# Optimization experiments

Measured on AMD Instinct MI355X. Metric: run time of the kernel, lower is better.

## Reference

```python
import jax, jax.numpy as jnp
import numpy as np

N_NODES = 100000
K_HOPS = 3  # PyG TAGConv default


def _gcn_norm(edge_index, num_nodes):
    # Symmetric normalization WITHOUT self-loops (TAGConv default).
    row, col = edge_index[0], edge_index[1]
    ones = jnp.ones(row.shape[0], dtype=jnp.float32)
    deg = jax.ops.segment_sum(ones, col, num_segments=num_nodes)
    dinv = jnp.where(deg > 0, jax.lax.rsqrt(jnp.maximum(deg, 1.0)), 0.0)
    return dinv[row] * dinv[col]


def _tagconv(x, row, col, norm, W, b, num_nodes):
    # out = Linear(concat_{k=0..K} (D^-1/2 A D^-1/2)^k x)
    xs = [x]
    h = x
    for _ in range(K_HOPS):
        h = jax.ops.segment_sum(norm[:, None] * h[row], col, num_segments=num_nodes)
        xs.append(h)
    return jnp.concatenate(xs, axis=-1) @ W.T + b


def setup_inputs() -> dict:
    key = jax.random.key(0)
    k1, k2, k3, k4, k5 = jax.random.split(key, 5)
    in_c, hid_c, out_c = 128, 128, 128
    n_edges = 1600000
    x = jax.random.normal(k1, (N_NODES, in_c), dtype=jnp.float32)
    edge_index = jax.random.randint(k2, (2, n_edges), 0, N_NODES, dtype=jnp.int64)
    s1 = 1.0 / np.sqrt(in_c * (K_HOPS + 1))
    s2 = 1.0 / np.sqrt(hid_c * (K_HOPS + 1))
    W1 = jax.random.normal(k3, (hid_c, in_c * (K_HOPS + 1)), dtype=jnp.float32) * s1
    b1 = jnp.zeros((hid_c,), dtype=jnp.float32)
    W2 = jax.random.normal(k4, (out_c, hid_c * (K_HOPS + 1)), dtype=jnp.float32) * s2
    b2 = jnp.zeros((out_c,), dtype=jnp.float32)
    return {"x": x, "edge_index": edge_index, "W1": W1, "b1": b1, "W2": W2, "b2": b2}


def reference(x, edge_index, W1, b1, W2, b2):
    row, col = edge_index[0], edge_index[1]
    norm = _gcn_norm(edge_index, N_NODES)  # [E]
    h = jax.nn.relu(_tagconv(x, row, col, norm, W1, b1, N_NODES))
    out = _tagconv(h, row, col, norm, W2, b2, N_NODES)
    return out.reshape(-1)  # original: x.view(n_nodes * out_channels)
```

## Files before the change

### kernel.cpp

```cpp
#include <hip/hip_runtime.h>
#include <hip/hip_fp16.h>

#define FEAT 128
#define BSH 8
#define BSZ 256
#define NBMAX 400
#define ABLK 4096
#define CAP 6144

typedef _Float16 half_t;
typedef _Float16 half4 __attribute__((ext_vector_type(4)));
typedef _Float16 half8 __attribute__((ext_vector_type(8)));
typedef float float4v __attribute__((ext_vector_type(4)));

__global__ void binit_kernel(int* __restrict__ gcur, int NB) {
    int b = blockIdx.x * blockDim.x + threadIdx.x;
    if (b < NB) gcur[b * 16] = b * CAP;
}

__global__ __launch_bounds__(256) void bucketA_kernel(const int* __restrict__ row,
                                                      const int* __restrict__ col,
                                                      int* __restrict__ gcur,
                                                      long long* __restrict__ tmp,
                                                      int E, int NB) {
    __shared__ int hist[NBMAX];
    __shared__ int gbase[NBMAX];
    int t = threadIdx.x;
    int base = blockIdx.x * ABLK;
    for (int i = t; i < NB; i += 256) hist[i] = 0;
    __syncthreads();
    int r[16], c[16];
#pragma unroll
    for (int j = 0; j < 16; ++j) {
        int e = base + j * 256 + t;
        if (e < E) {
            r[j] = __builtin_nontemporal_load(row + e);
            c[j] = __builtin_nontemporal_load(col + e);
            atomicAdd(&hist[c[j] >> BSH], 1);
        } else c[j] = -1;
    }
    __syncthreads();
    for (int b = t; b < NB; b += 256) {
        int cnt = hist[b];
        if (cnt > 0) gbase[b] = atomicAdd(&gcur[b * 16], cnt);
    }
    __syncthreads();
    for (int i = t; i < NB; i += 256) hist[i] = 0;
    __syncthreads();
#pragma unroll
    for (int j = 0; j < 16; ++j) {
        if (c[j] >= 0) {
            int b = c[j] >> BSH;
            int lpos = atomicAdd(&hist[b], 1);
            long long pk = ((long long)(unsigned)c[j] << 32) | (unsigned)r[j];
            tmp[gbase[b] + lpos] = pk;
        }
    }
}

__global__ __launch_bounds__(512) void bscan_kernel(const int* __restrict__ gcur,
                                                    int* __restrict__ bbase,
                                                    int* __restrict__ offsN, int NB) {
    __shared__ int sd[512];
    int t = threadIdx.x;
    int v = (t < NB) ? (gcur[t * 16] - t * CAP) : 0;
    sd[t] = v;
    __syncthreads();
    for (int o = 1; o < 512; o <<= 1) {
        int u = (t >= o) ? sd[t - o] : 0;
        __syncthreads();
        sd[t] += u;
        __syncthreads();
    }
    if (t < NB) bbase[t] = sd[t] - v;
    if (t == NB - 1) *offsN = sd[t];
}

__global__ __launch_bounds__(256) void bdeg_kernel(const long long* __restrict__ tmp,
                                                   const int* __restrict__ gcur,
                                                   const int* __restrict__ bbase,
                                                   int* __restrict__ offs,
                                                   float* __restrict__ dinv, int N) {
    __shared__ int ldeg[BSZ];
    __shared__ int sums[BSZ];
    int b = blockIdx.x;
    int lo = b << BSH;
    int t = threadIdx.x;
    int cnt = gcur[b * 16] - b * CAP;
    ldeg[t] = 0;
    __syncthreads();
    const long long* reg = tmp + (size_t)b * CAP;
    for (int i = t; i < cnt; i += 256) {
        int c = (int)(__builtin_nontemporal_load(reg + i) >> 32);
        atomicAdd(&ldeg[c - lo], 1);
    }
    __syncthreads();
    int d = ldeg[t];
    sums[t] = d;
    __syncthreads();
    for (int o = 1; o < 256; o <<= 1) {
        int u = (t >= o) ? sums[t - o] : 0;
        __syncthreads();
        sums[t] += u;
        __syncthreads();
    }
    int node = lo + t;
    if (node < N) {
        offs[node] = bbase[b] + sums[t] - d;
        dinv[node] = (d > 0) ? rsqrtf((float)d) : 0.0f;
    }
}

__global__ __launch_bounds__(256) void bplace_kernel(const long long* __restrict__ tmp,
                                                     const int* __restrict__ gcur,
                                                     const int* __restrict__ offs,
                                                     const float* __restrict__ dinv,
                                                     int2* __restrict__ csr, int N) {
    __shared__ int lcur[BSZ];
    int b = blockIdx.x;
    int lo = b << BSH;
    int hi = lo + BSZ;
    if (hi > N) hi = N;
    int t = threadIdx.x;
    int cnt = gcur[b * 16] - b * CAP;
    if (t < hi - lo) lcur[t] = offs[lo + t];
    __syncthreads();
    const long long* reg = tmp + (size_t)b * CAP;
    for (int i = t; i < cnt; i += 256) {
        long long pk = __builtin_nontemporal_load(reg + i);
        int r = (int)(pk & 0xffffffffLL);
        int c = (int)(pk >> 32);
        int pos = atomicAdd(&lcur[c - lo], 1);
        float w = dinv[r] * dinv[c];
        int2 o;
        o.x = r;
        o.y = __float_as_int(w);
        csr[pos] = o;
    }
}

__global__ void f2h3_kernel(const float* __restrict__ a, half_t* __restrict__ ah, int na4,
                            const float* __restrict__ b, half_t* __restrict__ bh, int nb4,
                            const float* __restrict__ c, half_t* __restrict__ ch, int nc4) {
    int i = blockIdx.x * blockDim.x + threadIdx.x;
    const float* src;
    half_t* dst;
    int j = i;
    if (j < na4) { src = a; dst = ah; }
    else if ((j -= na4) < nb4) { src = b; dst = bh; }
    else if ((j -= nb4) < nc4) { src = c; dst = ch; }
    else return;
    float4 v = ((const float4*)src)[j];
    half4 o;
    o.x = (half_t)v.x; o.y = (half_t)v.y; o.z = (half_t)v.z; o.w = (half_t)v.w;
    ((half4*)dst)[j] = o;
}

__global__ __launch_bounds__(256) void prop16_kernel(const half_t* __restrict__ src,
                                                     half_t* __restrict__ dst,
                                                     const int* __restrict__ offs,
                                                     const long long* __restrict__ csr, int N) {
    int v = blockIdx.x * 4 + (threadIdx.x >> 6);
    if (v >= N) return;
    int lane = threadIdx.x & 63;
    int q = lane >> 4;
    int p = lane & 15;
    int s0 = offs[v];
    int s1 = offs[v + 1];
    float acc[8];
#pragma unroll
    for (int j = 0; j < 8; ++j) acc[j] = 0.0f;

    for (int base = s0; base < s1; base += 8) {
        int i0 = base + q;
        int i1 = base + 4 + q;
        long long pk0 = (i0 < s1) ? __builtin_nontemporal_load(csr + i0) : 0LL;
        long long pk1 = (i1 < s1) ? __builtin_nontemporal_load(csr + i1) : 0LL;
        int r0 = (int)(pk0 & 0xffffffffLL);
        int r1 = (int)(pk1 & 0xffffffffLL);
        float w0 = __int_as_float((int)(pk0 >> 32));
        float w1 = __int_as_float((int)(pk1 >> 32));
        half8 va = *(const half8*)(src + (size_t)r0 * FEAT + p * 8);
        half8 vb = *(const half8*)(src + (size_t)r1 * FEAT + p * 8);
#pragma unroll
        for (int j = 0; j < 8; ++j) {
            acc[j] = fmaf(w0, (float)va[j], acc[j]);
            acc[j] = fmaf(w1, (float)vb[j], acc[j]);
        }
    }
#pragma unroll
    for (int j = 0; j < 8; ++j) {
        acc[j] += __shfl_xor(acc[j], 32, 64);
        acc[j] += __shfl_xor(acc[j], 16, 64);
    }
    if (lane < 16) {
        half8 o;
#pragma unroll
        for (int j = 0; j < 8; ++j) o[j] = (half_t)acc[j];
        *(half8*)(dst + (size_t)v * FEAT + p * 8) = o;
    }
}

template <bool RELU, bool HALFOUT>
__global__ __launch_bounds__(256) void gemm16_kernel(const half_t* __restrict__ H0,
                                                     const half_t* __restrict__ H1,
                                                     const half_t* __restrict__ H2,
                                                     const half_t* __restrict__ H3,
                                                     const half_t* __restrict__ W,
                                                     const float* __restrict__ bias,
                                                     half_t* __restrict__ out_h,
                                                     float* __restrict__ out_f, int N) {
    __shared__ half_t ws[128][40];
    const int tid = threadIdx.x;
    const int lane = tid & 63;
    const int wid = tid >> 6;
    const int lr = lane & 15;
    const int lk = lane >> 4;
    const int m = blockIdx.x * 64 + wid * 16 + lr;
    const bool mok = (m < N);

    float4v acc[8];
#pragma unroll
    for (int ct = 0; ct < 8; ++ct) acc[ct] = (float4v)0.0f;

    const half_t* Hs[4] = {H0, H1, H2, H3};
    const int wo = tid >> 1;
    const int wh = tid & 1;

#pragma unroll
    for (int b = 0; b < 4; ++b) {
        const half_t* __restrict__ H = Hs[b];
#pragma unroll
        for (int kt = 0; kt < 128; kt += 32) {
            half8 hfrag = (half8)(half_t)0.0f;
            if (mok) hfrag = *(const half8*)(H + (size_t)m * FEAT + kt + lk * 8);
            const half8* wsrc = (const half8*)(W + (size_t)wo * 512 + b * 128 + kt + wh * 16);
            half8 w0 = wsrc[0];
            half8 w1 = wsrc[1];
            __syncthreads();
            *(half8*)&ws[wo][wh * 16 + 0] = w0;
            *(half8*)&ws[wo][wh * 16 + 8] = w1;
            __syncthreads();
#pragma unroll
            for (int ct = 0; ct < 8; ++ct) {
                half8 wfrag = *(const half8*)&ws[ct * 16 + lr][lk * 8];
                acc[ct] = __builtin_amdgcn_mfma_f32_16x16x32_f16(wfrag, hfrag, acc[ct], 0, 0, 0);
            }
        }
    }

    if (mok) {
#pragma unroll
        for (int ct = 0; ct < 8; ++ct) {
            int o = ct * 16 + lk * 4;
            float4 bv = *(const float4*)(bias + o);
            float r0 = acc[ct][0] + bv.x;
            float r1 = acc[ct][1] + bv.y;
            float r2 = acc[ct][2] + bv.z;
            float r3 = acc[ct][3] + bv.w;
            if (RELU) {
                r0 = fmaxf(r0, 0.0f); r1 = fmaxf(r1, 0.0f);
                r2 = fmaxf(r2, 0.0f); r3 = fmaxf(r3, 0.0f);
            }
            if (HALFOUT) {
                half4 hv;
                hv.x = (half_t)r0; hv.y = (half_t)r1; hv.z = (half_t)r2; hv.w = (half_t)r3;
                *(half4*)(out_h + (size_t)m * FEAT + o) = hv;
            } else {
                float4 fv;
                fv.x = r0; fv.y = r1; fv.z = r2; fv.w = r3;
                *(float4*)(out_f + (size_t)m * FEAT + o) = fv;
            }
        }
    }
}

extern "C" void kernel_launch(void* const* d_in, const int* in_sizes, int n_in,
                              void* d_out, int out_size, void* d_ws, size_t ws_size,
                              hipStream_t stream) {
    const float* x   = (const float*)d_in[0];
    const int*   ei  = (const int*)d_in[1];
    const float* W1  = (const float*)d_in[2];
    const float* b1  = (const float*)d_in[3];
    const float* W2  = (const float*)d_in[4];
    const float* b2  = (const float*)d_in[5];
    float* out = (float*)d_out;

    const int N = in_sizes[0] / FEAT;
    const int E = in_sizes[1] / 2;
    const int* row = ei;
    const int* col = ei + E;
    const int NB = (N + BSZ - 1) / BSZ;

    size_t off = 0;
    auto carve = [&](size_t bytes) -> void* {
        void* p = (char*)d_ws + off;
        off += (bytes + 255) & ~(size_t)255;
        return p;
    };
    float*     dinv = (float*)carve((size_t)N * 4);
    int*       offs = (int*)carve((size_t)(N + 1) * 4);
    int*       bbase = (int*)carve((size_t)NB * 4);
    int*       gcur = (int*)carve((size_t)NB * 16 * 4);
    long long* tmp  = (long long*)carve((size_t)NB * CAP * 8);
    int2*      csr  = (int2*)carve((size_t)E * 8);
    half_t*    x16  = (half_t*)carve((size_t)N * FEAT * 2);
    half_t*    t1   = (half_t*)carve((size_t)N * FEAT * 2);
    half_t*    t2   = (half_t*)carve((size_t)N * FEAT * 2);
    half_t*    t3   = (half_t*)carve((size_t)N * FEAT * 2);
    half_t*    hbuf = (half_t*)carve((size_t)N * FEAT * 2);
    half_t*    w1h  = (half_t*)carve((size_t)FEAT * 512 * 2);
    half_t*    w2h  = (half_t*)carve((size_t)FEAT * 512 * 2);

    const int tB = 256;
    const int gA = (E + ABLK - 1) / ABLK;
    const int gP = (N + 3) / 4;
    const int gG = (N + 63) / 64;
    const int xt4 = N * FEAT / 4;
    const int wt4 = FEAT * 512 / 4;
    const int cvt_total = xt4 + 2 * wt4;

    binit_kernel<<<(NB + tB - 1) / tB, tB, 0, stream>>>(gcur, NB);
    bucketA_kernel<<<gA, 256, 0, stream>>>(row, col, gcur, tmp, E, NB);
    bscan_kernel<<<1, 512, 0, stream>>>(gcur, bbase, offs + N, NB);
    bdeg_kernel<<<NB, 256, 0, stream>>>(tmp, gcur, bbase, offs, dinv, N);
    bplace_kernel<<<NB, 256, 0, stream>>>(tmp, gcur, offs, dinv, csr, N);

    f2h3_kernel<<<(cvt_total + tB - 1) / tB, tB, 0, stream>>>(x, x16, xt4, W1, w1h, wt4, W2, w2h, wt4);

    const long long* csrll = (const long long*)csr;

    prop16_kernel<<<gP, 256, 0, stream>>>(x16, t1, offs, csrll, N);
    prop16_kernel<<<gP, 256, 0, stream>>>(t1, t2, offs, csrll, N);
    prop16_kernel<<<gP, 256, 0, stream>>>(t2, t3, offs, csrll, N);
    gemm16_kernel<true, true><<<gG, 256, 0, stream>>>(x16, t1, t2, t3, w1h, b1, hbuf, nullptr, N);

    prop16_kernel<<<gP, 256, 0, stream>>>(hbuf, t1, offs, csrll, N);
    prop16_kernel<<<gP, 256, 0, stream>>>(t1, t2, offs, csrll, N);
    prop16_kernel<<<gP, 256, 0, stream>>>(t2, t3, offs, csrll, N);
    gemm16_kernel<false, false><<<gG, 256, 0, stream>>>(hbuf, t1, t2, t3, w2h, b2, nullptr, out, N);
}
```

Before: 525.8 us.

## Split sparse propagation into two feature-half passes for cache locality

Result: slower. 761.7 us (+44.9%).

```diff
diff --git a/kernel.cpp b/kernel.cpp
--- a/kernel.cpp
+++ b/kernel.cpp
@@ -159,12 +159,13 @@
 __global__ __launch_bounds__(256) void prop16_kernel(const half_t* __restrict__ src,
                                                      half_t* __restrict__ dst,
                                                      const int* __restrict__ offs,
-                                                     const long long* __restrict__ csr, int N) {
+                                                     const long long* __restrict__ csr,
+                                                     int N, int d0) {
     int v = blockIdx.x * 4 + (threadIdx.x >> 6);
     if (v >= N) return;
     int lane = threadIdx.x & 63;
-    int q = lane >> 4;
-    int p = lane & 15;
+    int q = lane >> 3;
+    int p = lane & 7;
     int s0 = offs[v];
     int s1 = offs[v + 1];
     float acc[8];
@@ -173,31 +174,26 @@
 
     for (int base = s0; base < s1; base += 8) {
         int i0 = base + q;
-        int i1 = base + 4 + q;
         long long pk0 = (i0 < s1) ? __builtin_nontemporal_load(csr + i0) : 0LL;
-        long long pk1 = (i1 < s1) ? __builtin_nontemporal_load(csr + i1) : 0LL;
         int r0 = (int)(pk0 & 0xffffffffLL);
-        int r1 = (int)(pk1 & 0xffffffffLL);
         float w0 = __int_as_float((int)(pk0 >> 32));
-        float w1 = __int_as_float((int)(pk1 >> 32));
-        half8 va = *(const half8*)(src + (size_t)r0 * FEAT + p * 8);
-        half8 vb = *(const half8*)(src + (size_t)r1 * FEAT + p * 8);
+        half8 va = *(const half8*)(src + (size_t)r0 * FEAT + d0 + p * 8);
 #pragma unroll
         for (int j = 0; j < 8; ++j) {
             acc[j] = fmaf(w0, (float)va[j], acc[j]);
-            acc[j] = fmaf(w1, (float)vb[j], acc[j]);
         }
     }
 #pragma unroll
     for (int j = 0; j < 8; ++j) {
         acc[j] += __shfl_xor(acc[j], 32, 64);
         acc[j] += __shfl_xor(acc[j], 16, 64);
-    }
-    if (lane < 16) {
+        acc[j] += __shfl_xor(acc[j], 8, 64);
+    }
+    if (lane < 8) {
         half8 o;
 #pragma unroll
         for (int j = 0; j < 8; ++j) o[j] = (half_t)acc[j];
-        *(half8*)(dst + (size_t)v * FEAT + p * 8) = o;
+        *(half8*)(dst + (size_t)v * FEAT + d0 + p * 8) = o;
     }
 }
 
@@ -330,13 +326,18 @@
 
     const long long* csrll = (const long long*)csr;
 
-    prop16_kernel<<<gP, 256, 0, stream>>>(x16, t1, offs, csrll, N);
-    prop16_kernel<<<gP, 256, 0, stream>>>(t1, t2, offs, csrll, N);
-    prop16_kernel<<<gP, 256, 0, stream>>>(t2, t3, offs, csrll, N);
+    auto prop = [&](const half_t* s, half_t* d) {
+        prop16_kernel<<<gP, 256, 0, stream>>>(s, d, offs, csrll, N, 0);
+        prop16_kernel<<<gP, 256, 0, stream>>>(s, d, offs, csrll, N, 64);
+    };
+
+    prop(x16, t1);
+    prop(t1, t2);
+    prop(t2, t3);
     gemm16_kernel<true, true><<<gG, 256, 0, stream>>>(x16, t1, t2, t3, w1h, b1, hbuf, nullptr, N);
 
-    prop16_kernel<<<gP, 256, 0, stream>>>(hbuf, t1, offs, csrll, N);
-    prop16_kernel<<<gP, 256, 0, stream>>>(t1, t2, offs, csrll, N);
-    prop16_kernel<<<gP, 256, 0, stream>>>(t2, t3, offs, csrll, N);
+    prop(hbuf, t1);
+    prop(t1, t2);
+    prop(t2, t3);
     gemm16_kernel<false, false><<<gG, 256, 0, stream>>>(hbuf, t1, t2, t3, w2h, b2, nullptr, out, N);
 }
```

## Fold edge normalization into node-side dinv scaling and gather with unweighted fp16 sums

Applied to the files above, without the earlier changes.

Result: faster. 509.5 us (-3.1%).

```diff
diff --git a/kernel.cpp b/kernel.cpp
--- a/kernel.cpp
+++ b/kernel.cpp
@@ -114,8 +114,7 @@
 __global__ __launch_bounds__(256) void bplace_kernel(const long long* __restrict__ tmp,
                                                      const int* __restrict__ gcur,
                                                      const int* __restrict__ offs,
-                                                     const float* __restrict__ dinv,
-                                                     int2* __restrict__ csr, int N) {
+                                                     int* __restrict__ csr, int N) {
     __shared__ int lcur[BSZ];
     int b = blockIdx.x;
     int lo = b << BSH;
@@ -131,23 +130,39 @@
         int r = (int)(pk & 0xffffffffLL);
         int c = (int)(pk >> 32);
         int pos = atomicAdd(&lcur[c - lo], 1);
-        float w = dinv[r] * dinv[c];
-        int2 o;
-        o.x = r;
-        o.y = __float_as_int(w);
-        csr[pos] = o;
-    }
-}
-
-__global__ void f2h3_kernel(const float* __restrict__ a, half_t* __restrict__ ah, int na4,
+        csr[pos] = r;
+    }
+}
+
+__global__ void zrow_kernel(half_t* a, half_t* b, half_t* c, half_t* d, half_t* e, int N) {
+    int t = threadIdx.x;
+    size_t o = (size_t)N * FEAT + t;
+    a[o] = (half_t)0.0f; b[o] = (half_t)0.0f; c[o] = (half_t)0.0f;
+    d[o] = (half_t)0.0f; e[o] = (half_t)0.0f;
+}
+
+__global__ void f2h3_kernel(const float* __restrict__ a, half_t* __restrict__ ah,
+                            half_t* __restrict__ gh, const float* __restrict__ dinv, int na4,
                             const float* __restrict__ b, half_t* __restrict__ bh, int nb4,
                             const float* __restrict__ c, half_t* __restrict__ ch, int nc4) {
     int i = blockIdx.x * blockDim.x + threadIdx.x;
+    int j = i;
+    if (j < na4) {
+        float4 v = ((const float4*)a)[j];
+        half4 o;
+        o.x = (half_t)v.x; o.y = (half_t)v.y; o.z = (half_t)v.z; o.w = (half_t)v.w;
+        ((half4*)ah)[j] = o;
+        float dv = dinv[j >> 5];
+        half4 g;
+        g.x = (half_t)(v.x * dv); g.y = (half_t)(v.y * dv);
+        g.z = (half_t)(v.z * dv); g.w = (half_t)(v.w * dv);
+        ((half4*)gh)[j] = g;
+        return;
+    }
+    j -= na4;
     const float* src;
     half_t* dst;
-    int j = i;
-    if (j < na4) { src = a; dst = ah; }
-    else if ((j -= na4) < nb4) { src = b; dst = bh; }
+    if (j < nb4) { src = b; dst = bh; }
     else if ((j -= nb4) < nc4) { src = c; dst = ch; }
     else return;
     float4 v = ((const float4*)src)[j];
@@ -159,7 +174,8 @@
 __global__ __launch_bounds__(256) void prop16_kernel(const half_t* __restrict__ src,
                                                      half_t* __restrict__ dst,
                                                      const int* __restrict__ offs,
-                                                     const long long* __restrict__ csr, int N) {
+                                                     const int* __restrict__ csr,
+                                                     const float* __restrict__ dinv, int N) {
     int v = blockIdx.x * 4 + (threadIdx.x >> 6);
     if (v >= N) return;
     int lane = threadIdx.x & 63;
@@ -167,37 +183,48 @@
     int p = lane & 15;
     int s0 = offs[v];
     int s1 = offs[v + 1];
-    float acc[8];
-#pragma unroll
-    for (int j = 0; j < 8; ++j) acc[j] = 0.0f;
-
-    for (int base = s0; base < s1; base += 8) {
-        int i0 = base + q;
-        int i1 = base + 4 + q;
-        long long pk0 = (i0 < s1) ? __builtin_nontemporal_load(csr + i0) : 0LL;
-        long long pk1 = (i1 < s1) ? __builtin_nontemporal_load(csr + i1) : 0LL;
-        int r0 = (int)(pk0 & 0xffffffffLL);
-        int r1 = (int)(pk1 & 0xffffffffLL);
-        float w0 = __int_as_float((int)(pk0 >> 32));
-        float w1 = __int_as_float((int)(pk1 >> 32));
-        half8 va = *(const half8*)(src + (size_t)r0 * FEAT + p * 8);
-        half8 vb = *(const half8*)(src + (size_t)r1 * FEAT + p * 8);
-#pragma unroll
-        for (int j = 0; j < 8; ++j) {
-            acc[j] = fmaf(w0, (float)va[j], acc[j]);
-            acc[j] = fmaf(w1, (float)vb[j], acc[j]);
+    int last = s1 - 1;
+    half8 accA = (half8)(half_t)0.0f;
+    half8 accB = (half8)(half_t)0.0f;
+    for (int base = s0; base < s1; base += 32) {
+        int rr[8];
+#pragma unroll
+        for (int k = 0; k < 8; ++k) {
+            int i = base + k * 4 + q;
+            int ic = (i < s1) ? i : last;
+            int r = __builtin_nontemporal_load(csr + ic);
+            rr[k] = (i < s1) ? r : N;
         }
-    }
-#pragma unroll
-    for (int j = 0; j < 8; ++j) {
-        acc[j] += __shfl_xor(acc[j], 32, 64);
-        acc[j] += __shfl_xor(acc[j], 16, 64);
-    }
+        half8 g0 = *(const half8*)(src + (size_t)rr[0] * FEAT + p * 8);
+        half8 g1 = *(const half8*)(src + (size_t)rr[1] * FEAT + p * 8);
+        half8 g2 = *(const half8*)(src + (size_t)rr[2] * FEAT + p * 8);
+        half8 g3 = *(const half8*)(src + (size_t)rr[3] * FEAT + p * 8);
+        half8 g4 = *(const half8*)(src + (size_t)rr[4] * FEAT + p * 8);
+        half8 g5 = *(const half8*)(src + (size_t)rr[5] * FEAT + p * 8);
+        half8 g6 = *(const half8*)(src + (size_t)rr[6] * FEAT + p * 8);
+        half8 g7 = *(const half8*)(src + (size_t)rr[7] * FEAT + p * 8);
+        accA = accA + g0; accB = accB + g1;
+        accA = accA + g2; accB = accB + g3;
+        accA = accA + g4; accB = accB + g5;
+        accA = accA + g6; accB = accB + g7;
+    }
+    half8 acc = accA + accB;
+    union U { half8 h; int i[4]; };
+    U u, o1;
+    u.h = acc;
+#pragma unroll
+    for (int k = 0; k < 4; ++k) o1.i[k] = __shfl_xor(u.i[k], 32, 64);
+    u.h = u.h + o1.h;
+#pragma unroll
+    for (int k = 0; k < 4; ++k) o1.i[k] = __shfl_xor(u.i[k], 16, 64);
+    u.h = u.h + o1.h;
     if (lane < 16) {
-        half8 o;
-#pragma unroll
-        for (int j = 0; j < 8; ++j) o[j] = (half_t)acc[j];
-        *(half8*)(dst + (size_t)v * FEAT + p * 8) = o;
+        float d = dinv[v];
+        float d2 = d * d;
+        half8 outv;
+#pragma unroll
+        for (int j = 0; j < 8; ++j) outv[j] = (half_t)((float)u.h[j] * d2);
+        *(half8*)(dst + (size_t)v * FEAT + p * 8) = outv;
     }
 }
 
@@ -208,7 +235,9 @@
                                                      const half_t* __restrict__ H3,
                                                      const half_t* __restrict__ W,
                                                      const float* __restrict__ bias,
+                                                     const float* __restrict__ dinv,
                                                      half_t* __restrict__ out_h,
+                                                     half_t* __restrict__ gout,
                                                      float* __restrict__ out_f, int N) {
     __shared__ half_t ws[128][40];
     const int tid = threadIdx.x;
@@ -219,6 +248,9 @@
     const int m = blockIdx.x * 64 + wid * 16 + lr;
     const bool mok = (m < N);
 
+    float dm = mok ? dinv[m] : 0.0f;
+    half_t hs = (half_t)((dm > 0.0f) ? 1.0f / dm : 0.0f);
+
     float4v acc[8];
 #pragma unroll
     for (int ct = 0; ct < 8; ++ct) acc[ct] = (float4v)0.0f;
@@ -234,6 +266,7 @@
         for (int kt = 0; kt < 128; kt += 32) {
             half8 hfrag = (half8)(half_t)0.0f;
             if (mok) hfrag = *(const half8*)(H + (size_t)m * FEAT + kt + lk * 8);
+            if (b > 0) hfrag = hfrag * hs;
             const half8* wsrc = (const half8*)(W + (size_t)wo * 512 + b * 128 + kt + wh * 16);
             half8 w0 = wsrc[0];
             half8 w1 = wsrc[1];
@@ -250,6 +283,7 @@
     }
 
     if (mok) {
+        half_t hd = (half_t)dm;
 #pragma unroll
         for (int ct = 0; ct < 8; ++ct) {
             int o = ct * 16 + lk * 4;
@@ -266,6 +300,8 @@
                 half4 hv;
                 hv.x = (half_t)r0; hv.y = (half_t)r1; hv.z = (half_t)r2; hv.w = (half_t)r3;
                 *(half4*)(out_h + (size_t)m * FEAT + o) = hv;
+                half4 gv = hv * hd;
+                *(half4*)(gout + (size_t)m * FEAT + o) = gv;
             } else {
                 float4 fv;
                 fv.x = r0; fv.y = r1; fv.z = r2; fv.w = r3;
@@ -298,19 +334,21 @@
         off += (bytes + 255) & ~(size_t)255;
         return p;
     };
-    float*     dinv = (float*)carve((size_t)N * 4);
-    int*       offs = (int*)carve((size_t)(N + 1) * 4);
+    float*     dinv  = (float*)carve((size_t)N * 4);
+    int*       offs  = (int*)carve((size_t)(N + 1) * 4);
     int*       bbase = (int*)carve((size_t)NB * 4);
-    int*       gcur = (int*)carve((size_t)NB * 16 * 4);
-    long long* tmp  = (long long*)carve((size_t)NB * CAP * 8);
-    int2*      csr  = (int2*)carve((size_t)E * 8);
-    half_t*    x16  = (half_t*)carve((size_t)N * FEAT * 2);
-    half_t*    t1   = (half_t*)carve((size_t)N * FEAT * 2);
-    half_t*    t2   = (half_t*)carve((size_t)N * FEAT * 2);
-    half_t*    t3   = (half_t*)carve((size_t)N * FEAT * 2);
-    half_t*    hbuf = (half_t*)carve((size_t)N * FEAT * 2);
-    half_t*    w1h  = (half_t*)carve((size_t)FEAT * 512 * 2);
-    half_t*    w2h  = (half_t*)carve((size_t)FEAT * 512 * 2);
+    int*       gcur  = (int*)carve((size_t)NB * 16 * 4);
+    long long* tmp   = (long long*)carve((size_t)NB * CAP * 8);
+    int*       csr   = (int*)carve((size_t)(E + 64) * 4);
+    half_t*    x16   = (half_t*)carve((size_t)N * FEAT * 2);
+    half_t*    g0    = (half_t*)carve((size_t)(N + 1) * FEAT * 2);
+    half_t*    t1    = (half_t*)carve((size_t)(N + 1) * FEAT * 2);
+    half_t*    t2    = (half_t*)carve((size_t)(N + 1) * FEAT * 2);
+    half_t*    t3    = (half_t*)carve((size_t)(N + 1) * FEAT * 2);
+    half_t*    hbuf  = (half_t*)carve((size_t)N * FEAT * 2);
+    half_t*    ghbuf = (half_t*)carve((size_t)(N + 1) * FEAT * 2);
+    half_t*    w1h   = (half_t*)carve((size_t)FEAT * 512 * 2);
+    half_t*    w2h   = (half_t*)carve((size_t)FEAT * 512 * 2);
 
     const int tB = 256;
     const int gA = (E + ABLK - 1) / ABLK;
@@ -324,19 +362,21 @@
     bucketA_kernel<<<gA, 256, 0, stream>>>(row, col, gcur, tmp, E, NB);
     bscan_kernel<<<1, 512, 0, stream>>>(gcur, bbase, offs + N, NB);
     bdeg_kernel<<<NB, 256, 0, stream>>>(tmp, gcur, bbase, offs, dinv, N);
-    bplace_kernel<<<NB, 256, 0, stream>>>(tmp, gcur, offs, dinv, csr, N);
-
-    f2h3_kernel<<<(cvt_total + tB - 1) / tB, tB, 0, stream>>>(x, x16, xt4, W1, w1h, wt4, W2, w2h, wt4);
-
-    const long long* csrll = (const long long*)csr;
-
-    prop16_kernel<<<gP, 256, 0, stream>>>(x16, t1, offs, csrll, N);
-    prop16_kernel<<<gP, 256, 0, stream>>>(t1, t2, offs, csrll, N);
-    prop16_kernel<<<gP, 256, 0, stream>>>(t2, t3, offs, csrll, N);
-    gemm16_kernel<true, true><<<gG, 256, 0, stream>>>(x16, t1, t2, t3, w1h, b1, hbuf, nullptr, N);
-
-    prop16_kernel<<<gP, 256, 0, stream>>>(hbuf, t1, offs, csrll, N);
-    prop16_kernel<<<gP, 256, 0, stream>>>(t1, t2, offs, csrll, N);
-    prop16_kernel<<<gP, 256, 0, stream>>>(t2, t3, offs, csrll, N);
-    gemm16_kernel<false, false><<<gG, 256, 0, stream>>>(hbuf, t1, t2, t3, w2h, b2, nullptr, out, N);
-}
+    bplace_kernel<<<NB, 256, 0, stream>>>(tmp, gcur, offs, csr, N);
+
+    zrow_kernel<<<1, 128, 0, stream>>>(g0, t1, t2, t3, ghbuf, N);
+    f2h3_kernel<<<(cvt_total + tB - 1) / tB, tB, 0, stream>>>(x, x16, g0, dinv, xt4,
+                                                              W1, w1h, wt4, W2, w2h, wt4);
+
+    prop16_kernel<<<gP, 256, 0, stream>>>(g0, t1, offs, csr, dinv, N);
+    prop16_kernel<<<gP, 256, 0, stream>>>(t1, t2, offs, csr, dinv, N);
+    prop16_kernel<<<gP, 256, 0, stream>>>(t2, t3, offs, csr, dinv, N);
+    gemm16_kernel<true, true><<<gG, 256, 0, stream>>>(x16, t1, t2, t3, w1h, b1, dinv,
+                                                      hbuf, ghbuf, nullptr, N);
+
+    prop16_kernel<<<gP, 256, 0, stream>>>(ghbuf, t1, offs, csr, dinv, N);
+    prop16_kernel<<<gP, 256, 0, stream>>>(t1, t2, offs, csr, dinv, N);
+    prop16_kernel<<<gP, 256, 0, stream>>>(t2, t3, offs, csr, dinv, N);
+    gemm16_kernel<false, false><<<gG, 256, 0, stream>>>(hbuf, t1, t2, t3, w2h, b2, dinv,
+                                                        nullptr, nullptr, out, N);
+}
```
